# Kernel tuning notes

Hardware: AMD Instinct MI355X
Metric: run time of the kernel (lower is better)

Reference implementation:

```python
import jax, jax.numpy as jnp
import numpy as np

VOCAB = 100000
SIDE = 50000
D = 128
BS = 16384


def setup_inputs() -> dict:
    key = jax.random.key(0)
    ks = jax.random.split(key, 10)
    x = jax.random.randint(ks[0], (BS, 1, 3), 0, SIDE, dtype=jnp.int64) if jax.config.jax_enable_x64 else jax.random.randint(ks[0], (BS, 1, 3), 0, SIDE, dtype=jnp.int32)
    s = 0.02
    return {
        "x": x,
        "tgt_base": jax.random.normal(ks[1], (VOCAB, D), jnp.float32) * s,
        "tgt_a": jax.random.normal(ks[2], (SIDE, D), jnp.float32) * s,
        "tgt_b": jax.random.normal(ks[3], (SIDE, D), jnp.float32) * s,
        "ctx_base": jax.random.normal(ks[4], (VOCAB, D), jnp.float32) * s,
        "ctx_a": jax.random.normal(ks[5], (SIDE, D), jnp.float32) * s,
        "ctx_b": jax.random.normal(ks[6], (SIDE, D), jnp.float32) * s,
        "tgt_w": jax.random.normal(ks[7], (3, 1), jnp.float32),
        "ctx_w": jax.random.normal(ks[8], (3, 1), jnp.float32),
    }


def _weighted_embed(idx, tables, weights):
    # idx: (bs, 3); tables: list of 3 (N_i, D); weights: (3, 1)
    emb = jnp.stack([tables[i][idx[:, i]] for i in range(3)], axis=1)  # (bs, 3, D)
    w = jax.nn.softmax(weights, axis=0)  # (3, 1)
    return jnp.einsum('bnd,nl->bld', emb, w)  # (bs, 1, D)


def reference(x, tgt_base, tgt_a, tgt_b, ctx_base, ctx_a, ctx_b, tgt_w, ctx_w):
    target_idx = x[:, 0, :]   # (bs, 3)
    context_idx = x[:, 0, :]  # same slice, as in original forward
    tgt = _weighted_embed(target_idx, [tgt_base, tgt_a, tgt_b], tgt_w)   # (bs, 1, D)
    ctx = _weighted_embed(context_idx, [ctx_base, ctx_a, ctx_b], ctx_w)  # (bs, 1, D)
    logits = jnp.matmul(tgt, jnp.swapaxes(ctx, 1, 2))  # (bs, 1, 1)
    return jax.nn.sigmoid(logits).squeeze()  # (bs,)
```

## Files before the change

kernel.cpp:

```cpp
#include <hip/hip_runtime.h>
#include <hip/hip_bf16.h>
#include <math.h>


#define D 128
#define WAVES_PER_BLOCK 4

__global__ __launch_bounds__(64 * WAVES_PER_BLOCK)
void sgns_kernel(const int* __restrict__ x,
                 const float* __restrict__ tgt_base,
                 const float* __restrict__ tgt_a,
                 const float* __restrict__ tgt_b,
                 const float* __restrict__ ctx_base,
                 const float* __restrict__ ctx_a,
                 const float* __restrict__ ctx_b,
                 const float* __restrict__ tgt_w,
                 const float* __restrict__ ctx_w,
                 float* __restrict__ out,
                 int bs) {
    const int wave = threadIdx.x >> 6;
    const int lane = threadIdx.x & 63;
    const int b = blockIdx.x * WAVES_PER_BLOCK + wave;
    if (b >= bs) return;

    float t0 = tgt_w[0], t1 = tgt_w[1], t2 = tgt_w[2];
    float tm = fmaxf(t0, fmaxf(t1, t2));
    float te0 = __expf(t0 - tm), te1 = __expf(t1 - tm), te2 = __expf(t2 - tm);
    float tinv = 1.0f / (te0 + te1 + te2);
    float wt0 = te0 * tinv, wt1 = te1 * tinv, wt2 = te2 * tinv;

    float c0 = ctx_w[0], c1 = ctx_w[1], c2 = ctx_w[2];
    float cm = fmaxf(c0, fmaxf(c1, c2));
    float ce0 = __expf(c0 - cm), ce1 = __expf(c1 - cm), ce2 = __expf(c2 - cm);
    float cinv = 1.0f / (ce0 + ce1 + ce2);
    float wc0 = ce0 * cinv, wc1 = ce1 * cinv, wc2 = ce2 * cinv;

    const int i0 = x[b * 3 + 0];
    const int i1 = x[b * 3 + 1];
    const int i2 = x[b * 3 + 2];

    const float2* tb0 = (const float2*)(tgt_base + (size_t)i0 * D);
    const float2* tb1 = (const float2*)(tgt_a    + (size_t)i1 * D);
    const float2* tb2 = (const float2*)(tgt_b    + (size_t)i2 * D);
    const float2* cb0 = (const float2*)(ctx_base + (size_t)i0 * D);
    const float2* cb1 = (const float2*)(ctx_a    + (size_t)i1 * D);
    const float2* cb2 = (const float2*)(ctx_b    + (size_t)i2 * D);

    float2 ta = tb0[lane];
    float2 tbv = tb1[lane];
    float2 tc = tb2[lane];
    float2 ca = cb0[lane];
    float2 cbv = cb1[lane];
    float2 cc = cb2[lane];

    float tx = wt0 * ta.x + wt1 * tbv.x + wt2 * tc.x;
    float ty = wt0 * ta.y + wt1 * tbv.y + wt2 * tc.y;
    float cx = wc0 * ca.x + wc1 * cbv.x + wc2 * cc.x;
    float cy = wc0 * ca.y + wc1 * cbv.y + wc2 * cc.y;

    float p = tx * cx + ty * cy;

    #pragma unroll
    for (int off = 32; off > 0; off >>= 1)
        p += __shfl_down(p, off, 64);

    if (lane == 0)
        out[b] = 1.0f / (1.0f + __expf(-p));
}

extern "C" void kernel_launch(void* const* d_in, const int* in_sizes, int n_in,
                              void* d_out, int out_size, void* d_ws, size_t ws_size,
                              hipStream_t stream) {
    const int*   x        = (const int*)  d_in[0];
    const float* tgt_base = (const float*)d_in[1];
    const float* tgt_a    = (const float*)d_in[2];
    const float* tgt_b    = (const float*)d_in[3];
    const float* ctx_base = (const float*)d_in[4];
    const float* ctx_a    = (const float*)d_in[5];
    const float* ctx_b    = (const float*)d_in[6];
    const float* tgt_w    = (const float*)d_in[7];
    const float* ctx_w    = (const float*)d_in[8];
    float* out = (float*)d_out;

    const int bs = out_size;
    const int block = 64 * WAVES_PER_BLOCK;
    const int grid = (bs + WAVES_PER_BLOCK - 1) / WAVES_PER_BLOCK;

    sgns_kernel<<<grid, block, 0, stream>>>(x, tgt_base, tgt_a, tgt_b,
                                            ctx_base, ctx_a, ctx_b,
                                            tgt_w, ctx_w, out, bs);
}
```

Before: 175.1 us.

## Process four batch rows per wave with float4 gathers and half-wave reductions

Each wave now handles four batch elements: each half-wave of 32 lanes loads a full 128-float row using float4 loads, and it does this for two elements per half. All twelve row loads are issued before the softmax weights are computed, so more memory requests are in flight per thread. Reductions become 5-step shuffles within 32 lanes. The grid shrinks by a factor of four, which lowers the number of waves but raises per-thread memory-level parallelism.

```diff
diff --git a/kernel.cpp b/kernel.cpp
--- a/kernel.cpp
+++ b/kernel.cpp
@@ -5,6 +5,7 @@
 
 #define D 128
 #define WAVES_PER_BLOCK 4
+#define ELEMS_PER_WAVE 4
 
 __global__ __launch_bounds__(64 * WAVES_PER_BLOCK)
 void sgns_kernel(const int* __restrict__ x,
@@ -20,8 +21,34 @@
                  int bs) {
     const int wave = threadIdx.x >> 6;
     const int lane = threadIdx.x & 63;
-    const int b = blockIdx.x * WAVES_PER_BLOCK + wave;
-    if (b >= bs) return;
+    const int half = lane >> 5;
+    const int sub  = lane & 31;
+    const int b0 = (blockIdx.x * WAVES_PER_BLOCK + wave) * ELEMS_PER_WAVE;
+    if (b0 >= bs) return;
+
+    int j0[2], j1[2], j2[2], bsel[2];
+    #pragma unroll
+    for (int p = 0; p < 2; ++p) {
+        int b = b0 + 2 * p + half;
+        bsel[p] = b;
+        b = b < bs ? b : bs - 1;
+        const int* xp = x + (size_t)b * 3;
+        j0[p] = xp[0];
+        j1[p] = xp[1];
+        j2[p] = xp[2];
+    }
+
+    float4 T0[2], T1[2], T2[2], C0[2], C1[2], C2[2];
+    #pragma unroll
+    for (int p = 0; p < 2; ++p) {
+        const size_t off = (size_t)sub * 4;
+        T0[p] = *(const float4*)(tgt_base + (size_t)j0[p] * D + off);
+        T1[p] = *(const float4*)(tgt_a    + (size_t)j1[p] * D + off);
+        T2[p] = *(const float4*)(tgt_b    + (size_t)j2[p] * D + off);
+        C0[p] = *(const float4*)(ctx_base + (size_t)j0[p] * D + off);
+        C1[p] = *(const float4*)(ctx_a    + (size_t)j1[p] * D + off);
+        C2[p] = *(const float4*)(ctx_b    + (size_t)j2[p] * D + off);
+    }
 
     float t0 = tgt_w[0], t1 = tgt_w[1], t2 = tgt_w[2];
     float tm = fmaxf(t0, fmaxf(t1, t2));
@@ -35,37 +62,27 @@
     float cinv = 1.0f / (ce0 + ce1 + ce2);
     float wc0 = ce0 * cinv, wc1 = ce1 * cinv, wc2 = ce2 * cinv;
 
-    const int i0 = x[b * 3 + 0];
-    const int i1 = x[b * 3 + 1];
-    const int i2 = x[b * 3 + 2];
+    #pragma unroll
+    for (int p = 0; p < 2; ++p) {
+        float tx = wt0 * T0[p].x + wt1 * T1[p].x + wt2 * T2[p].x;
+        float ty = wt0 * T0[p].y + wt1 * T1[p].y + wt2 * T2[p].y;
+        float tz = wt0 * T0[p].z + wt1 * T1[p].z + wt2 * T2[p].z;
+        float tw = wt0 * T0[p].w + wt1 * T1[p].w + wt2 * T2[p].w;
 
-    const float2* tb0 = (const float2*)(tgt_base + (size_t)i0 * D);
-    const float2* tb1 = (const float2*)(tgt_a    + (size_t)i1 * D);
-    const float2* tb2 = (const float2*)(tgt_b    + (size_t)i2 * D);
-    const float2* cb0 = (const float2*)(ctx_base + (size_t)i0 * D);
-    const float2* cb1 = (const float2*)(ctx_a    + (size_t)i1 * D);
-    const float2* cb2 = (const float2*)(ctx_b    + (size_t)i2 * D);
+        float cx = wc0 * C0[p].x + wc1 * C1[p].x + wc2 * C2[p].x;
+        float cy = wc0 * C0[p].y + wc1 * C1[p].y + wc2 * C2[p].y;
+        float cz = wc0 * C0[p].z + wc1 * C1[p].z + wc2 * C2[p].z;
+        float cw = wc0 * C0[p].w + wc1 * C1[p].w + wc2 * C2[p].w;
 
-    float2 ta = tb0[lane];
-    float2 tbv = tb1[lane];
-    float2 tc = tb2[lane];
-    float2 ca = cb0[lane];
-    float2 cbv = cb1[lane];
-    float2 cc = cb2[lane];
+        float d = tx * cx + ty * cy + tz * cz + tw * cw;
 
-    float tx = wt0 * ta.x + wt1 * tbv.x + wt2 * tc.x;
-    float ty = wt0 * ta.y + wt1 * tbv.y + wt2 * tc.y;
-    float cx = wc0 * ca.x + wc1 * cbv.x + wc2 * cc.x;
-    float cy = wc0 * ca.y + wc1 * cbv.y + wc2 * cc.y;
+        #pragma unroll
+        for (int off = 16; off > 0; off >>= 1)
+            d += __shfl_down(d, off, 32);
 
-    float p = tx * cx + ty * cy;
-
-    #pragma unroll
-    for (int off = 32; off > 0; off >>= 1)
-        p += __shfl_down(p, off, 64);
-
-    if (lane == 0)
-        out[b] = 1.0f / (1.0f + __expf(-p));
+        if (sub == 0 && bsel[p] < bs)
+            out[bsel[p]] = 1.0f / (1.0f + __expf(-d));
+    }
 }
 
 extern "C" void kernel_launch(void* const* d_in, const int* in_sizes, int n_in,
@@ -83,8 +100,9 @@
     float* out = (float*)d_out;
 
     const int bs = out_size;
+    const int elems_per_block = WAVES_PER_BLOCK * ELEMS_PER_WAVE;
     const int block = 64 * WAVES_PER_BLOCK;
-    const int grid = (bs + WAVES_PER_BLOCK - 1) / WAVES_PER_BLOCK;
+    const int grid = (bs + elems_per_block - 1) / elems_per_block;
 
     sgns_kernel<<<grid, block, 0, stream>>>(x, tgt_base, tgt_a, tgt_b,
                                             ctx_base, ctx_a, ctx_b,
```

New measurement: 176.4 us. About the same (+0.7%).
